# Optimization experiments

Measured on AMD Instinct MI355X. Metric: run time of the kernel, lower is better.

## Reference

```python
import jax, jax.numpy as jnp
import numpy as np

NUM_HEADS = 16

def setup_inputs() -> dict:
    key = jax.random.key(0)
    k1, k2, k3 = jax.random.split(key, 3)
    B, N, C = 4, 2048, 1024
    x = jax.random.normal(k1, (B, N, C), dtype=jnp.float32)
    # torch Linear weights are [out_features, in_features]
    w_qkv = jax.random.normal(k2, (3 * C, C), dtype=jnp.float32) * (1.0 / np.sqrt(C))
    w_out = jax.random.normal(k3, (C, C), dtype=jnp.float32) * (1.0 / np.sqrt(C))
    b_out = jnp.zeros((C,), dtype=jnp.float32)
    return {"x": x, "w_qkv": w_qkv, "w_out": w_out, "b_out": b_out}

def reference(x, w_qkv, w_out, b_out):
    B, N, C = x.shape
    H = NUM_HEADS
    D = C // H
    scale = 1.0 / np.sqrt(D).astype(np.float32)
    # qkv projection: [B,N,3C] -> [3,B,H,N,D]
    qkv = (x @ w_qkv.T).reshape(B, N, 3, H, D).transpose(2, 0, 3, 1, 4)
    q, k, v = qkv[0], qkv[1], qkv[2]
    # The torch module's block-wise online softmax telescopes to exact softmax.
    scores = jnp.einsum("bhqd,bhkd->bhqk", q, k) * scale
    attn = jax.nn.softmax(scores, axis=-1)
    out = jnp.einsum("bhqk,bhkd->bhqd", attn, v)  # [B,H,N,D]
    out = out.transpose(0, 2, 1, 3).reshape(B, N, C)
    return out @ w_out.T + b_out
```

## Files before the change

### kernel.cpp

```cpp
#include <hip/hip_runtime.h>

typedef __attribute__((ext_vector_type(8))) short vbf8;
typedef __attribute__((ext_vector_type(4))) float vf4;

#define GLOAD16(g, l) __builtin_amdgcn_global_load_lds( \
    (const __attribute__((address_space(1))) void*)(g),  \
    (__attribute__((address_space(3))) void*)(l), 16, 0, 0)

__device__ __forceinline__ unsigned short f2bf(float f) {
  union { float f; unsigned u; } v; v.f = f;
  return (unsigned short)((v.u + 0x7fffu + ((v.u >> 16) & 1u)) >> 16);
}

__device__ __forceinline__ unsigned short cvt_bf16(float f) {
  __bf16 h = (__bf16)f;
  union { __bf16 h; unsigned short u; } v; v.h = h;
  return v.u;
}

__device__ __forceinline__ vf4 mfma16(vbf8 a, vbf8 b, vf4 c) {
  return __builtin_amdgcn_mfma_f32_16x16x32_bf16(a, b, c, 0, 0, 0);
}

__device__ __forceinline__ int swz(int row, int col) {
  return row * 64 + (col ^ ((row & 7) << 3));
}

__global__ __launch_bounds__(256)
void k_cvt_bf16(const float* __restrict__ in, unsigned short* __restrict__ out, int n4) {
  for (int i = blockIdx.x * blockDim.x + threadIdx.x; i < n4; i += gridDim.x * blockDim.x) {
    float4 v = ((const float4*)in)[i];
    ushort4 o;
    o.x = f2bf(v.x); o.y = f2bf(v.y); o.z = f2bf(v.z); o.w = f2bf(v.w);
    ((ushort4*)out)[i] = o;
  }
}

__global__ __launch_bounds__(256, 2)
void k_gemm_qkv(const unsigned short* __restrict__ A,
                const unsigned short* __restrict__ B,
                unsigned short* __restrict__ qb,
                unsigned short* __restrict__ kb,
                unsigned short* __restrict__ vb) {
  __shared__ unsigned short As[128 * 64];
  __shared__ unsigned short Bs[128 * 64];
  const int tid = threadIdx.x;
  const int lane = tid & 63;
  const int wid = tid >> 6;
  const int wm = wid >> 1, wn = wid & 1;
  const int flat = blockIdx.y * 24 + blockIdx.x;
  const int sw = (flat & 7) * 192 + (flat >> 3);
  const int m0 = (sw / 24) * 128;
  const int n0 = (sw % 24) * 128;
  const int l15 = lane & 15, kg = lane >> 4;
  const int srow = wid * 32 + (lane >> 3);
  const int scol = (lane & 7) * 8;

  vf4 acc[4][4] = {};

  for (int kt = 0; kt < 16; ++kt) {
    __syncthreads();
    const unsigned short* gA = A + (size_t)(m0 + srow) * 1024 + kt * 64 + scol;
    const unsigned short* gB = B + (size_t)(n0 + srow) * 1024 + kt * 64 + scol;
    const unsigned ab = (unsigned)(wid * 32 * 64);
#pragma unroll
    for (int i = 0; i < 4; ++i) {
      GLOAD16(gA + (size_t)i * 8 * 1024, &As[ab + i * 8 * 64]);
      GLOAD16(gB + (size_t)i * 8 * 1024, &Bs[ab + i * 8 * 64]);
    }
    __syncthreads();
#pragma unroll
    for (int kk = 0; kk < 2; ++kk) {
      vbf8 af[4], bfr[4];
#pragma unroll
      for (int mi = 0; mi < 4; ++mi)
        af[mi] = *(const vbf8*)&As[(wm * 64 + mi * 16 + l15) * 64 + kk * 32 + kg * 8];
#pragma unroll
      for (int ni = 0; ni < 4; ++ni)
        bfr[ni] = *(const vbf8*)&Bs[(wn * 64 + ni * 16 + l15) * 64 + kk * 32 + kg * 8];
#pragma unroll
      for (int mi = 0; mi < 4; ++mi)
#pragma unroll
        for (int ni = 0; ni < 4; ++ni)
          acc[mi][ni] = mfma16(af[mi], bfr[ni], acc[mi][ni]);
    }
  }

#pragma unroll
  for (int ni = 0; ni < 4; ++ni) {
    const int c = n0 + wn * 64 + ni * 16 + l15;
    const int which = c >> 10;
    const int hd = c & 1023;
    unsigned short* dst = (which == 0) ? qb : ((which == 1) ? kb : vb);
    const float sc = (which == 0) ? 0.18033688011112042f : 1.0f;
#pragma unroll
    for (int mi = 0; mi < 4; ++mi) {
#pragma unroll
      for (int r = 0; r < 4; ++r) {
        const int m = m0 + wm * 64 + mi * 16 + kg * 4 + r;
        const int b = m >> 11, nn = m & 2047;
        const size_t idx = (((size_t)(b * 16 + (hd >> 6)) * 2048 + nn) * 64) + (hd & 63);
        dst[idx] = f2bf(acc[mi][ni][r] * sc);
      }
    }
  }
}

__global__ __launch_bounds__(256)
void k_transpose_v(const unsigned short* __restrict__ vb, unsigned short* __restrict__ vt) {
  __shared__ unsigned short t[64][72];
  const int bh = blockIdx.y, n0 = blockIdx.x * 64;
  const int tid = threadIdx.x;
#pragma unroll
  for (int p = 0; p < 2; ++p) {
    const int r = p * 32 + (tid >> 3);
    vbf8 v = *(const vbf8*)&vb[((size_t)bh * 2048 + n0 + r) * 64 + (tid & 7) * 8];
    *(vbf8*)&t[r][(tid & 7) * 8] = v;
  }
  __syncthreads();
  const int d = tid >> 2, jb = (tid & 3) * 16;
  unsigned short buf[16];
#pragma unroll
  for (int j = 0; j < 16; ++j) buf[j] = t[jb + j][d];
  unsigned short* o = &vt[((size_t)bh * 64 + d) * 2048 + n0 + jb];
  *(vbf8*)&o[0] = *(vbf8*)&buf[0];
  *(vbf8*)&o[8] = *(vbf8*)&buf[8];
}

__global__ __launch_bounds__(256, 3)
void k_attn(const unsigned short* __restrict__ qb,
            const unsigned short* __restrict__ kb,
            const unsigned short* __restrict__ vt,
            unsigned short* __restrict__ ob) {
  __shared__ unsigned short Ks[2][64 * 64];
  __shared__ unsigned short Vs[2][64 * 64];
  __shared__ unsigned short Ps[4][32][72];
  const int tid = threadIdx.x, lane = tid & 63, w = tid >> 6;
  const int l15 = lane & 15, kg = lane >> 4;
  const int flat = blockIdx.x;
  const int sw = (flat & 7) * 128 + (flat >> 3);
  const int qt = sw & 15, bh = sw >> 4;

  const unsigned short* Q = qb + ((size_t)bh * 2048 + qt * 128 + w * 32) * 64;
  vbf8 qf[2][2];
#pragma unroll
  for (int qj = 0; qj < 2; ++qj)
#pragma unroll
    for (int kk = 0; kk < 2; ++kk)
      qf[qj][kk] = *(const vbf8*)(Q + (qj * 16 + l15) * 64 + kk * 32 + kg * 8);

  vbf8 onesv;
#pragma unroll
  for (int i = 0; i < 8; ++i) onesv[i] = (short)0x3F80;

  vf4 oacc[2][4] = {};
  vf4 lacc[2] = {};
  float mrun[2] = {-3.0e38f, -3.0e38f};

  const int srow = lane >> 3;
  const int scol = (((lane & 7) ^ srow) * 8);
  const unsigned short* gKbase = kb + ((size_t)bh * 2048 + w * 16 + srow) * 64 + scol;
  const unsigned short* gVbase = vt + ((size_t)bh * 64 + w * 16 + srow) * 2048 + scol;

#define STAGE(t, b) do { \
    const unsigned short* gK_ = gKbase + (size_t)(t) * 4096; \
    const unsigned short* gV_ = gVbase + (size_t)(t) * 64; \
    GLOAD16(gK_,                 &Ks[b][(w * 16) * 64]); \
    GLOAD16(gK_ + 512,           &Ks[b][(w * 16 + 8) * 64]); \
    GLOAD16(gV_,                 &Vs[b][(w * 16) * 64]); \
    GLOAD16(gV_ + (size_t)16384, &Vs[b][(w * 16 + 8) * 64]); \
  } while (0)

  STAGE(0, 0);
  __syncthreads();

  for (int kt = 0; kt < 32; ++kt) {
    const int cur = kt & 1;
    if (kt + 1 < 32) STAGE(kt + 1, cur ^ 1);

    vf4 s[2][4] = {};
    __builtin_amdgcn_s_setprio(1);
#pragma unroll
    for (int kk = 0; kk < 2; ++kk)
#pragma unroll
      for (int ni = 0; ni < 4; ++ni) {
        const vbf8 kf = *(const vbf8*)&Ks[cur][swz(ni * 16 + l15, kk * 32 + kg * 8)];
        s[0][ni] = mfma16(kf, qf[0][kk], s[0][ni]);
        s[1][ni] = mfma16(kf, qf[1][kk], s[1][ni]);
      }
    __builtin_amdgcn_s_setprio(0);

#pragma unroll
    for (int qj = 0; qj < 2; ++qj) {
      float a0 = fmaxf(fmaxf(s[qj][0][0], s[qj][0][1]), fmaxf(s[qj][0][2], s[qj][0][3]));
      float a1 = fmaxf(fmaxf(s[qj][1][0], s[qj][1][1]), fmaxf(s[qj][1][2], s[qj][1][3]));
      float a2 = fmaxf(fmaxf(s[qj][2][0], s[qj][2][1]), fmaxf(s[qj][2][2], s[qj][2][3]));
      float a3 = fmaxf(fmaxf(s[qj][3][0], s[qj][3][1]), fmaxf(s[qj][3][2], s[qj][3][3]));
      float rm = fmaxf(fmaxf(a0, a1), fmaxf(a2, a3));
      rm = fmaxf(rm, __shfl_xor(rm, 16));
      rm = fmaxf(rm, __shfl_xor(rm, 32));

      if (__any(rm > mrun[qj] + 8.0f)) {
        const float mn = fmaxf(mrun[qj], rm);
        const float alpha = __builtin_amdgcn_exp2f(mrun[qj] - mn);
        mrun[qj] = mn;
        float av[4];
#pragma unroll
        for (int r = 0; r < 4; ++r) av[r] = __shfl(alpha, kg * 4 + r);
#pragma unroll
        for (int r = 0; r < 4; ++r) {
          lacc[qj][r] *= av[r];
#pragma unroll
          for (int ni = 0; ni < 4; ++ni) oacc[qj][ni][r] *= av[r];
        }
      }

#pragma unroll
      for (int ni = 0; ni < 4; ++ni) {
        ushort4 pk;
        pk.x = cvt_bf16(__builtin_amdgcn_exp2f(s[qj][ni][0] - mrun[qj]));
        pk.y = cvt_bf16(__builtin_amdgcn_exp2f(s[qj][ni][1] - mrun[qj]));
        pk.z = cvt_bf16(__builtin_amdgcn_exp2f(s[qj][ni][2] - mrun[qj]));
        pk.w = cvt_bf16(__builtin_amdgcn_exp2f(s[qj][ni][3] - mrun[qj]));
        *(ushort4*)&Ps[w][qj * 16 + l15][ni * 16 + kg * 4] = pk;
      }
    }
    asm volatile("s_waitcnt lgkmcnt(0)" ::: "memory");

    __builtin_amdgcn_s_setprio(1);
#pragma unroll
    for (int kk = 0; kk < 2; ++kk) {
      const vbf8 pf0 = *(const vbf8*)&Ps[w][l15][kk * 32 + kg * 8];
      const vbf8 pf1 = *(const vbf8*)&Ps[w][16 + l15][kk * 32 + kg * 8];
      lacc[0] = mfma16(pf0, onesv, lacc[0]);
      lacc[1] = mfma16(pf1, onesv, lacc[1]);
#pragma unroll
      for (int ni = 0; ni < 4; ++ni) {
        const vbf8 vf = *(const vbf8*)&Vs[cur][swz(ni * 16 + l15, kk * 32 + kg * 8)];
        oacc[0][ni] = mfma16(pf0, vf, oacc[0][ni]);
        oacc[1][ni] = mfma16(pf1, vf, oacc[1][ni]);
      }
    }
    __builtin_amdgcn_s_setprio(0);

    __syncthreads();
  }
#undef STAGE

  const int b = bh >> 4, h = bh & 15;
#pragma unroll
  for (int qj = 0; qj < 2; ++qj)
#pragma unroll
    for (int r = 0; r < 4; ++r) {
      const float inv = 1.0f / lacc[qj][r];
      const int q = qt * 128 + w * 32 + qj * 16 + kg * 4 + r;
#pragma unroll
      for (int ni = 0; ni < 4; ++ni)
        ob[((size_t)b * 2048 + q) * 1024 + h * 64 + ni * 16 + l15] = cvt_bf16(oacc[qj][ni][r] * inv);
    }
}

__global__ __launch_bounds__(256, 2)
void k_gemm_out(const unsigned short* __restrict__ A,
                const unsigned short* __restrict__ B,
                const float* __restrict__ bias,
                float* __restrict__ out) {
  __shared__ unsigned short As[128 * 64];
  __shared__ unsigned short Bs[128 * 64];
  const int tid = threadIdx.x;
  const int lane = tid & 63;
  const int wid = tid >> 6;
  const int wm = wid >> 1, wn = wid & 1;
  const int flat = blockIdx.y * 8 + blockIdx.x;
  const int sw = (flat & 7) * 64 + (flat >> 3);
  const int m0 = (sw / 8) * 128;
  const int n0 = (sw % 8) * 128;
  const int l15 = lane & 15, kg = lane >> 4;
  const int srow = wid * 32 + (lane >> 3);
  const int scol = (lane & 7) * 8;

  vf4 acc[4][4] = {};

  for (int kt = 0; kt < 16; ++kt) {
    __syncthreads();
    const unsigned short* gA = A + (size_t)(m0 + srow) * 1024 + kt * 64 + scol;
    const unsigned short* gB = B + (size_t)(n0 + srow) * 1024 + kt * 64 + scol;
    const unsigned ab = (unsigned)(wid * 32 * 64);
#pragma unroll
    for (int i = 0; i < 4; ++i) {
      GLOAD16(gA + (size_t)i * 8 * 1024, &As[ab + i * 8 * 64]);
      GLOAD16(gB + (size_t)i * 8 * 1024, &Bs[ab + i * 8 * 64]);
    }
    __syncthreads();
#pragma unroll
    for (int kk = 0; kk < 2; ++kk) {
      vbf8 af[4], bfr[4];
#pragma unroll
      for (int mi = 0; mi < 4; ++mi)
        af[mi] = *(const vbf8*)&As[(wm * 64 + mi * 16 + l15) * 64 + kk * 32 + kg * 8];
#pragma unroll
      for (int ni = 0; ni < 4; ++ni)
        bfr[ni] = *(const vbf8*)&Bs[(wn * 64 + ni * 16 + l15) * 64 + kk * 32 + kg * 8];
#pragma unroll
      for (int mi = 0; mi < 4; ++mi)
#pragma unroll
        for (int ni = 0; ni < 4; ++ni)
          acc[mi][ni] = mfma16(af[mi], bfr[ni], acc[mi][ni]);
    }
  }

#pragma unroll
  for (int ni = 0; ni < 4; ++ni) {
    const int c = n0 + wn * 64 + ni * 16 + l15;
    const float bv = bias[c];
#pragma unroll
    for (int mi = 0; mi < 4; ++mi) {
#pragma unroll
      for (int r = 0; r < 4; ++r) {
        const int m = m0 + wm * 64 + mi * 16 + kg * 4 + r;
        out[(size_t)m * 1024 + c] = acc[mi][ni][r] + bv;
      }
    }
  }
}

extern "C" void kernel_launch(void* const* d_in, const int* in_sizes, int n_in,
                              void* d_out, int out_size, void* d_ws, size_t ws_size,
                              hipStream_t stream) {
  const float* x     = (const float*)d_in[0];
  const float* w_qkv = (const float*)d_in[1];
  const float* w_out = (const float*)d_in[2];
  const float* b_out = (const float*)d_in[3];
  float* out = (float*)d_out;

  char* ws = (char*)d_ws;
  unsigned short* xbf   = (unsigned short*)(ws);
  unsigned short* wqkvb = (unsigned short*)(ws + 16777216);
  unsigned short* woutb = (unsigned short*)(ws + 23068672);
  unsigned short* qbuf  = (unsigned short*)(ws + 25165824);
  unsigned short* kbuf  = (unsigned short*)(ws + 41943040);
  unsigned short* vbuf  = (unsigned short*)(ws + 58720256);
  unsigned short* vtbuf = (unsigned short*)(ws + 75497472);
  unsigned short* aob   = xbf;

  k_cvt_bf16<<<2048, 256, 0, stream>>>(x, xbf, 8388608 / 4);
  k_cvt_bf16<<<768, 256, 0, stream>>>(w_qkv, wqkvb, 3145728 / 4);
  k_cvt_bf16<<<256, 256, 0, stream>>>(w_out, woutb, 1048576 / 4);

  k_gemm_qkv<<<dim3(24, 64), 256, 0, stream>>>(xbf, wqkvb, qbuf, kbuf, vbuf);
  k_transpose_v<<<dim3(32, 64), 256, 0, stream>>>(vbuf, vtbuf);
  k_attn<<<dim3(1024), 256, 0, stream>>>(qbuf, kbuf, vtbuf, aob);
  k_gemm_out<<<dim3(8, 64), 256, 0, stream>>>(aob, woutb, b_out, out);
}
```

Before: 225.2 us.

## Single-buffer V tile, XOR-swizzle P scratch, raise attention occupancy to four blocks

The attention kernel now keeps K double-buffered but loads V into a single buffer at the start of each iteration, waiting for it with a vmcnt wait and barrier just before the PV matmul. The P scratch loses its padding and uses an XOR swizzle to avoid bank conflicts. The LDS footprint drops from about 50KB to about 40KB per block, so launch bounds go to 4 blocks per CU for more occupancy. The V load is now exposed within the iteration instead of being prefetched a full tile ahead, and the tighter register budget could cause spills.

```diff
diff --git a/kernel.cpp b/kernel.cpp
--- a/kernel.cpp
+++ b/kernel.cpp
@@ -127,14 +127,14 @@
   *(vbf8*)&o[8] = *(vbf8*)&buf[8];
 }
 
-__global__ __launch_bounds__(256, 3)
+__global__ __launch_bounds__(256, 4)
 void k_attn(const unsigned short* __restrict__ qb,
             const unsigned short* __restrict__ kb,
             const unsigned short* __restrict__ vt,
             unsigned short* __restrict__ ob) {
   __shared__ unsigned short Ks[2][64 * 64];
-  __shared__ unsigned short Vs[2][64 * 64];
-  __shared__ unsigned short Ps[4][32][72];
+  __shared__ unsigned short Vs[64 * 64];
+  __shared__ unsigned short Ps[4][32][64];
   const int tid = threadIdx.x, lane = tid & 63, w = tid >> 6;
   const int l15 = lane & 15, kg = lane >> 4;
   const int flat = blockIdx.x;
@@ -159,24 +159,30 @@
 
   const int srow = lane >> 3;
   const int scol = (((lane & 7) ^ srow) * 8);
+  const int pswz = (l15 & 7) << 3;
   const unsigned short* gKbase = kb + ((size_t)bh * 2048 + w * 16 + srow) * 64 + scol;
   const unsigned short* gVbase = vt + ((size_t)bh * 64 + w * 16 + srow) * 2048 + scol;
 
-#define STAGE(t, b) do { \
+#define STAGE_K(t, b) do { \
     const unsigned short* gK_ = gKbase + (size_t)(t) * 4096; \
+    GLOAD16(gK_,       &Ks[b][(w * 16) * 64]); \
+    GLOAD16(gK_ + 512, &Ks[b][(w * 16 + 8) * 64]); \
+  } while (0)
+#define STAGE_V(t) do { \
     const unsigned short* gV_ = gVbase + (size_t)(t) * 64; \
-    GLOAD16(gK_,                 &Ks[b][(w * 16) * 64]); \
-    GLOAD16(gK_ + 512,           &Ks[b][(w * 16 + 8) * 64]); \
-    GLOAD16(gV_,                 &Vs[b][(w * 16) * 64]); \
-    GLOAD16(gV_ + (size_t)16384, &Vs[b][(w * 16 + 8) * 64]); \
+    GLOAD16(gV_,                 &Vs[(w * 16) * 64]); \
+    GLOAD16(gV_ + (size_t)16384, &Vs[(w * 16 + 8) * 64]); \
   } while (0)
 
-  STAGE(0, 0);
-  __syncthreads();
+  STAGE_K(0, 0);
+  asm volatile("s_waitcnt vmcnt(0)" ::: "memory");
+  __builtin_amdgcn_s_barrier();
+  __builtin_amdgcn_sched_barrier(0);
 
   for (int kt = 0; kt < 32; ++kt) {
     const int cur = kt & 1;
-    if (kt + 1 < 32) STAGE(kt + 1, cur ^ 1);
+    STAGE_V(kt);
+    if (kt + 1 < 32) STAGE_K(kt + 1, cur ^ 1);
 
     vf4 s[2][4] = {};
     __builtin_amdgcn_s_setprio(1);
@@ -222,21 +228,25 @@
         pk.y = cvt_bf16(__builtin_amdgcn_exp2f(s[qj][ni][1] - mrun[qj]));
         pk.z = cvt_bf16(__builtin_amdgcn_exp2f(s[qj][ni][2] - mrun[qj]));
         pk.w = cvt_bf16(__builtin_amdgcn_exp2f(s[qj][ni][3] - mrun[qj]));
-        *(ushort4*)&Ps[w][qj * 16 + l15][ni * 16 + kg * 4] = pk;
-      }
-    }
-    asm volatile("s_waitcnt lgkmcnt(0)" ::: "memory");
+        *(ushort4*)&Ps[w][qj * 16 + l15][(ni * 16 + kg * 4) ^ pswz] = pk;
+      }
+    }
+
+    if (kt + 1 < 32) asm volatile("s_waitcnt vmcnt(2) lgkmcnt(0)" ::: "memory");
+    else             asm volatile("s_waitcnt vmcnt(0) lgkmcnt(0)" ::: "memory");
+    __builtin_amdgcn_s_barrier();
+    __builtin_amdgcn_sched_barrier(0);
 
     __builtin_amdgcn_s_setprio(1);
 #pragma unroll
     for (int kk = 0; kk < 2; ++kk) {
-      const vbf8 pf0 = *(const vbf8*)&Ps[w][l15][kk * 32 + kg * 8];
-      const vbf8 pf1 = *(const vbf8*)&Ps[w][16 + l15][kk * 32 + kg * 8];
+      const vbf8 pf0 = *(const vbf8*)&Ps[w][l15][(kk * 32 + kg * 8) ^ pswz];
+      const vbf8 pf1 = *(const vbf8*)&Ps[w][16 + l15][(kk * 32 + kg * 8) ^ pswz];
       lacc[0] = mfma16(pf0, onesv, lacc[0]);
       lacc[1] = mfma16(pf1, onesv, lacc[1]);
 #pragma unroll
       for (int ni = 0; ni < 4; ++ni) {
-        const vbf8 vf = *(const vbf8*)&Vs[cur][swz(ni * 16 + l15, kk * 32 + kg * 8)];
+        const vbf8 vf = *(const vbf8*)&Vs[swz(ni * 16 + l15, kk * 32 + kg * 8)];
         oacc[0][ni] = mfma16(pf0, vf, oacc[0][ni]);
         oacc[1][ni] = mfma16(pf1, vf, oacc[1][ni]);
       }
@@ -245,7 +255,8 @@
 
     __syncthreads();
   }
-#undef STAGE
+#undef STAGE_K
+#undef STAGE_V
 
   const int b = bh >> 4, h = bh & 15;
 #pragma unroll
```

New measurement: 215.4 us. 4.4% less time.
